# Kernel tuning notes

Measured on AMD Instinct MI355X. Metric: run time of the kernel, lower is better.

## Reference

```python
import jax, jax.numpy as jnp
import numpy as np

SOC, EOS = 3, 2
NUM_HEADS = 12
LN_EPS = 1e-5


def setup_inputs() -> dict:
    key = jax.random.key(0)
    ks = jax.random.split(key, 24)
    B, S, D, N, FF, K = 8, 4096, 768, 1024, 3072, 640
    img = jax.random.normal(ks[0], (B, N, D), jnp.float32)
    hid = jax.random.normal(ks[1], (B, S, D), jnp.float32)
    seq = jax.random.randint(ks[2], (B, S), 4, 100)
    m = jax.random.uniform(ks[3], (B, S)) < 0.125
    seq = jnp.where(m, SOC, seq).at[:, 0].set(SOC)  # ensure >=1 SOC per row
    w = lambda k, a, b: jax.random.normal(k, (a, b), jnp.float32) * 0.02
    return {
        "img": img, "hid": hid, "seq": seq,
        "wq_s": w(ks[4], D, D), "wk_s": w(ks[5], D, D), "wv_s": w(ks[6], D, D), "wo_s": w(ks[7], D, D),
        "wq_c": w(ks[8], D, D), "wk_c": w(ks[9], D, D), "wv_c": w(ks[10], D, D), "wo_c": w(ks[11], D, D),
        "w_ff1": w(ks[12], D, FF), "w_ff2": w(ks[13], FF, D),
        "ln1_s": jnp.ones((D,)), "ln1_b": jnp.zeros((D,)),
        "ln2_s": jnp.ones((D,)), "ln2_b": jnp.zeros((D,)),
        "ln3_s": jnp.ones((D,)), "ln3_b": jnp.zeros((D,)),
        "cap": K,
    }


def _ln(x, s, b):
    mu = jnp.mean(x, axis=-1, keepdims=True)
    var = jnp.var(x, axis=-1, keepdims=True)
    return (x - mu) * jax.lax.rsqrt(var + LN_EPS) * s + b


def _mha(q_in, kv_in, wq, wk, wv, wo, key_mask):
    # q_in [B,Lq,D], kv_in [B,Lk,D], key_mask [B,Lk] bool or None
    B, Lq, D = q_in.shape
    H = NUM_HEADS
    dh = D // H
    q = (q_in @ wq).reshape(B, Lq, H, dh)
    k = (kv_in @ wk).reshape(B, -1, H, dh)
    v = (kv_in @ wv).reshape(B, -1, H, dh)
    scores = jnp.einsum("bqhd,bkhd->bhqk", q, k) / np.sqrt(dh).astype(q.dtype)
    if key_mask is not None:
        scores = jnp.where(key_mask[:, None, None, :], scores, jnp.asarray(-1e9, scores.dtype))
    att = jax.nn.softmax(scores, axis=-1)
    out = jnp.einsum("bhqk,bkhd->bqhd", att, v).reshape(B, Lq, D)
    return out @ wo


def _extract(data, mask, cap):
    # data [B,S,...], mask [B,S] bool -> packed+zero-padded [B,cap,...]
    pos = jnp.cumsum(mask, axis=1) - 1          # slot for each valid token
    pos = jnp.where(mask, pos, cap)             # invalid tokens -> dump slot
    def one(d, p):
        buf = jnp.zeros((cap + 1,) + d.shape[1:], d.dtype)
        return buf.at[p].set(d)[:cap]
        # note: dump slot cap is sliced away
    return jax.vmap(one)(data, pos), pos


def reference(img, hid, seq, wq_s, wk_s, wv_s, wo_s, wq_c, wk_c, wv_c, wo_c,
              w_ff1, w_ff2, ln1_s, ln1_b, ln2_s, ln2_b, ln3_s, ln3_b, cap):
    # mask: SOC tokens occurring before the first EOS
    soc = (seq == SOC) & (jnp.cumsum(seq == EOS, axis=1) == 0)  # [B,S]
    ext, pos = _extract(hid, soc, cap)                          # [B,K,D]
    counts = jnp.sum(soc, axis=1)                               # [B]
    run = jnp.arange(cap)[None, :] < counts[:, None]            # [B,K] valid slots

    # Blocks: pre-LN self-attn (key mask = run), cross-attn to img, FFN
    x = ext
    x = x + _mha(_ln(x, ln1_s, ln1_b), _ln(x, ln1_s, ln1_b), wq_s, wk_s, wv_s, wo_s, run)
    x = x + _mha(_ln(x, ln2_s, ln2_b), img, wq_c, wk_c, wv_c, wo_c, None)
    h = _ln(x, ln3_s, ln3_b)
    x = x + jax.nn.gelu(h @ w_ff1) @ w_ff2

    # masked_scatter back: each SOC position (b,s) takes x[b, pos[b,s]]
    idx = jnp.clip(pos, 0, cap - 1)
    gathered = jnp.take_along_axis(x, idx[:, :, None], axis=1)  # [B,S,D]
    hid_new = jnp.where(soc[:, :, None], gathered, hid)
    return hid_new, x
```

## Files before the change

### kernel.cpp

```cpp
#include <hip/hip_runtime.h>
#include <hip/hip_bf16.h>


#define B_    8
#define S_    4096
#define D_    768
#define N_    1024
#define FF_   3072
#define H_    12
#define DH_   64
#define KCAP  640
#define SOC_TOK 3
#define EOS_TOK 2

typedef __hip_bfloat16 bf16;
typedef unsigned short u16;
typedef __attribute__((ext_vector_type(8))) short short8;
typedef __attribute__((ext_vector_type(4))) float f32x4;

__device__ __forceinline__ u16 ftou16(float x){ union{bf16 b; u16 s;} c; c.b = __float2bfloat16(x); return c.s; }
__device__ __forceinline__ unsigned pk2(float lo, float hi){ return (unsigned)ftou16(lo) | ((unsigned)ftou16(hi)<<16); }

__device__ __forceinline__ f32x4 MFMA(short8 a, short8 b, f32x4 c){
  return __builtin_amdgcn_mfma_f32_16x16x32_bf16(a, b, c, 0, 0, 0);
}

__device__ __forceinline__ void gld16(const void* gp, void* lp){
  __builtin_amdgcn_global_load_lds(
    reinterpret_cast<const __attribute__((address_space(1))) unsigned int*>((size_t)gp),
    reinterpret_cast<__attribute__((address_space(3))) unsigned int*>((size_t)lp),
    16, 0, 0);
}

template<int N> __device__ __forceinline__ void vwait(){
  asm volatile("s_waitcnt vmcnt(%0)" :: "i"(N) : "memory");
}
__device__ __forceinline__ void wgbar(){ asm volatile("s_barrier" ::: "memory"); }

__device__ __forceinline__ int xcd_swz(){
  int id = blockIdx.x;
  return (id & 7) * ((int)gridDim.x >> 3) + (id >> 3);
}

__device__ void scan_body(const int* __restrict__ seq, int* __restrict__ pos,
                          int* __restrict__ src, int* __restrict__ counts, int b){
  int tid = threadIdx.x;
  __shared__ int sd[256];
  __shared__ int carryE, carryS;
  if (tid==0){ carryE=0; carryS=0; }
  __syncthreads();
  for (int c=0; c<S_; c+=256){
    int s   = c + tid;
    int tok = seq[b*S_ + s];
    int isE = (tok==EOS_TOK) ? 1 : 0;
    int isS = (tok==SOC_TOK) ? 1 : 0;
    sd[tid]=isE; __syncthreads();
    for (int off=1; off<256; off<<=1){ int t_=(tid>=off)?sd[tid-off]:0; __syncthreads(); sd[tid]+=t_; __syncthreads(); }
    int eIncl = sd[tid];
    int eTot  = sd[255];
    int valid = (isS && (carryE + eIncl)==0) ? 1 : 0;
    __syncthreads();
    sd[tid]=valid; __syncthreads();
    for (int off=1; off<256; off<<=1){ int t_=(tid>=off)?sd[tid-off]:0; __syncthreads(); sd[tid]+=t_; __syncthreads(); }
    int vIncl = sd[tid];
    int vTot  = sd[255];
    if (valid){
      int slot = carryS + vIncl - 1;
      pos[b*S_ + s] = slot;
      if (slot < KCAP) src[b*KCAP + slot] = s;
    } else {
      pos[b*S_ + s] = -1;
    }
    __syncthreads();
    if (tid==0){ carryE += eTot; carryS += vTot; }
    __syncthreads();
  }
  if (tid==0) counts[b] = (carryS < KCAP) ? carryS : KCAP;
}

struct TransArgs { const float* w[10]; u16* o[10]; };
__global__ __launch_bounds__(256) void transpose_scan_k(TransArgs a, const int* __restrict__ seq,
                                                        int* __restrict__ pos, int* __restrict__ src,
                                                        int* __restrict__ counts,
                                                        const float* __restrict__ img, u16* __restrict__ imgB){
  int id = blockIdx.x;
  if (id >= 9224){
    int base = (id - 9224)*2048 + threadIdx.x*8;
    float4 a0 = *(const float4*)(img + base);
    float4 a1 = *(const float4*)(img + base + 4);
    uint4 wv;
    wv.x = pk2(a0.x,a0.y); wv.y = pk2(a0.z,a0.w); wv.z = pk2(a1.x,a1.y); wv.w = pk2(a1.z,a1.w);
    *(uint4*)(imgB + base) = wv;
    return;
  }
  if (id >= 9216){ scan_body(seq, pos, src, counts, id - 9216); return; }
  __shared__ float tile[32][33];
  int wi, t, K, N;
  if (id < 4608){ wi = id/576; t = id%576; K = 768; N = 768; }
  else if (id < 6912){ wi = 8; t = id-4608; K = 768; N = 3072; }
  else { wi = 9; t = id-6912; K = 3072; N = 768; }
  const float* in = a.w[wi]; u16* out = a.o[wi];
  int nbx = N >> 5;
  int bx = t % nbx, by = t / nbx;
  int tx = threadIdx.x & 31, ty = threadIdx.x >> 5;
  #pragma unroll
  for (int i=0;i<4;++i)
    tile[ty + i*8][tx] = in[(size_t)(by*32 + ty + i*8)*N + bx*32 + tx];
  __syncthreads();
  #pragma unroll
  for (int i=0;i<4;++i)
    out[(size_t)(bx*32 + ty + i*8)*K + by*32 + tx] = ftou16(tile[tx][ty + i*8]);
}

__global__ __launch_bounds__(256) void gather_ln_k(const float* __restrict__ hid,
                                                   const int* __restrict__ src,
                                                   const int* __restrict__ counts,
                                                   const float* __restrict__ g, const float* __restrict__ bt,
                                                   float* __restrict__ X, u16* __restrict__ T0){
  int bk = blockIdx.x; int b = bk / KCAP; int k = bk % KCAP;
  int tid = threadIdx.x;
  float v0, v1, v2;
  if (k < counts[b]){
    const float* hr = hid + ((size_t)b*S_ + src[b*KCAP + k])*D_;
    v0 = hr[tid]; v1 = hr[tid+256]; v2 = hr[tid+512];
  } else { v0 = v1 = v2 = 0.f; }
  float* xr = X + (size_t)bk*D_;
  xr[tid] = v0; xr[tid+256] = v1; xr[tid+512] = v2;
  float s1=v0+v1+v2, s2=v0*v0+v1*v1+v2*v2;
  for (int off=32; off; off>>=1){ s1+=__shfl_xor(s1,off); s2+=__shfl_xor(s2,off); }
  __shared__ float red[8];
  __shared__ float mu_s, rs_s;
  int w=tid>>6, ln=tid&63;
  if (ln==0){ red[w]=s1; red[4+w]=s2; }
  __syncthreads();
  if (tid==0){
    float S1=red[0]+red[1]+red[2]+red[3];
    float S2=red[4]+red[5]+red[6]+red[7];
    float mu = S1*(1.f/D_);
    float var= S2*(1.f/D_) - mu*mu;
    mu_s=mu; rs_s=rsqrtf(var + 1e-5f);
  }
  __syncthreads();
  float mu=mu_s, rs=rs_s;
  u16* yr = T0 + (size_t)bk*D_;
  yr[tid]     = ftou16((v0-mu)*rs*g[tid]     + bt[tid]);
  yr[tid+256] = ftou16((v1-mu)*rs*g[tid+256] + bt[tid+256]);
  yr[tid+512] = ftou16((v2-mu)*rs*g[tid+512] + bt[tid+512]);
}

__global__ __launch_bounds__(256) void ln_k(const float* __restrict__ X, u16* __restrict__ Y,
                                            const float* __restrict__ g, const float* __restrict__ bt){
  int r = blockIdx.x; int tid = threadIdx.x;
  const float* xr = X + (size_t)r*D_;
  float v0=xr[tid], v1=xr[tid+256], v2=xr[tid+512];
  float s1=v0+v1+v2, s2=v0*v0+v1*v1+v2*v2;
  for (int off=32; off; off>>=1){ s1+=__shfl_xor(s1,off); s2+=__shfl_xor(s2,off); }
  __shared__ float red[8];
  __shared__ float mu_s, rs_s;
  int w=tid>>6, ln=tid&63;
  if (ln==0){ red[w]=s1; red[4+w]=s2; }
  __syncthreads();
  if (tid==0){
    float S1=red[0]+red[1]+red[2]+red[3];
    float S2=red[4]+red[5]+red[6]+red[7];
    float mu = S1*(1.f/D_);
    float var= S2*(1.f/D_) - mu*mu;
    mu_s=mu; rs_s=rsqrtf(var + 1e-5f);
  }
  __syncthreads();
  float mu=mu_s, rs=rs_s;
  u16* yr = Y + (size_t)r*D_;
  yr[tid]     = ftou16((v0-mu)*rs*g[tid]     + bt[tid]);
  yr[tid+256] = ftou16((v1-mu)*rs*g[tid+256] + bt[tid+256]);
  yr[tid+512] = ftou16((v2-mu)*rs*g[tid+512] + bt[tid+512]);
}

template<int MODE, int BM, typename TA>
__device__ __forceinline__ void gemm_body(char* ldsp, const TA* __restrict__ A, const u16* __restrict__ Bt,
                                          void* __restrict__ C0, void* __restrict__ C1, void* __restrict__ C2,
                                          int wgid, int N, int K){
  constexpr int MI   = BM/32;
  constexpr int NBUF = (BM==128) ? 2 : ((sizeof(TA)==4) ? 2 : 3);
  u16* As = (u16*)ldsp;
  u16* Bs = (u16*)(ldsp + NBUF*(BM*32)*2);
  int nbx = N >> 7;
  int bx = wgid % nbx, by = wgid / nbx;
  int tid = threadIdx.x;
  int w = tid>>6, l = tid&63, g = l>>4, c = l&15;
  int wr = w&1, wc = w>>1;
  f32x4 acc[MI][4] = {};
  float4 rg[4];
  const int NK = K/32;

  auto STAGEB = [&](int buf, int kt){
    #pragma unroll
    for (int p=0;p<2;++p){
      int row = w*32 + p*16 + (l>>2);
      int su  = (l&3) ^ ((row>>1)&3);
      gld16((const void*)(Bt + (size_t)(bx*128+row)*K + kt + su*8), (void*)&Bs[buf*128*32 + (w*32+p*16)*32]);
    }
  };
  auto STAGEA16 = [&](int buf, int kt){
    if constexpr (BM==128){
      #pragma unroll
      for (int p=0;p<2;++p){
        int row = w*32 + p*16 + (l>>2);
        int su  = (l&3) ^ ((row>>1)&3);
        gld16((const void*)((const u16*)A + (size_t)(by*BM+row)*K + kt + su*8), (void*)&As[buf*BM*32 + (w*32+p*16)*32]);
      }
    } else {
      int row = w*16 + (l>>2);
      int su  = (l&3) ^ ((row>>1)&3);
      gld16((const void*)((const u16*)A + (size_t)(by*BM+row)*K + kt + su*8), (void*)&As[buf*BM*32 + (w*16)*32]);
    }
  };
  auto LOADREG = [&](int kt){
    if constexpr (BM==128){
      const float* ap = (const float*)A + (size_t)(by*BM + (tid>>1))*K + kt + (tid&1)*16;
      rg[0]=*(const float4*)ap;     rg[1]=*(const float4*)(ap+4);
      rg[2]=*(const float4*)(ap+8); rg[3]=*(const float4*)(ap+12);
    } else {
      const float* ap = (const float*)A + (size_t)(by*BM + (tid>>2))*K + kt + (tid&3)*8;
      rg[0] = *(const float4*)ap; rg[1] = *(const float4*)(ap+4);
    }
  };
  auto WRITEA = [&](int buf){
    if constexpr (BM==128){
      int row = tid>>1, half = tid&1;
      uint4 w0,w1;
      w0.x=pk2(rg[0].x,rg[0].y); w0.y=pk2(rg[0].z,rg[0].w); w0.z=pk2(rg[1].x,rg[1].y); w0.w=pk2(rg[1].z,rg[1].w);
      w1.x=pk2(rg[2].x,rg[2].y); w1.y=pk2(rg[2].z,rg[2].w); w1.z=pk2(rg[3].x,rg[3].y); w1.w=pk2(rg[3].z,rg[3].w);
      int sw = (row>>1)&3;
      *(uint4*)&As[buf*BM*32 + row*32 + ((half*2  )^sw)*8] = w0;
      *(uint4*)&As[buf*BM*32 + row*32 + ((half*2+1)^sw)*8] = w1;
    } else {
      int row = tid>>2, unit = tid&3;
      uint4 wv;
      wv.x=pk2(rg[0].x,rg[0].y); wv.y=pk2(rg[0].z,rg[0].w); wv.z=pk2(rg[1].x,rg[1].y); wv.w=pk2(rg[1].z,rg[1].w);
      int sw = (row>>1)&3;
      *(uint4*)&As[buf*BM*32 + row*32 + (unit^sw)*8] = wv;
    }
  };
  auto COMPUTE = [&](int buf){
    short8 af[MI], bfr[4];
    #pragma unroll
    for (int mi=0;mi<MI;++mi){ int row = wr*(MI*16) + mi*16 + c; af[mi]  = *(const short8*)&As[buf*BM*32 + row*32 + (g^((row>>1)&3))*8]; }
    #pragma unroll
    for (int ni=0;ni<4;++ni){ int row = wc*64 + ni*16 + c;       bfr[ni] = *(const short8*)&Bs[buf*128*32 + row*32 + (g^((row>>1)&3))*8]; }
    #pragma unroll
    for (int mi=0;mi<MI;++mi)
      #pragma unroll
      for (int ni=0;ni<4;++ni) acc[mi][ni] = MFMA(af[mi], bfr[ni], acc[mi][ni]);
  };

  if constexpr (BM==128 || sizeof(TA)==4){
    if constexpr (sizeof(TA)==4){ LOADREG(0); STAGEB(0,0); WRITEA(0); }
    else { STAGEA16(0,0); STAGEB(0,0); }
    __syncthreads();
    int buf = 0;
    for (int t=0;t<NK;++t){
      int ktn = (t+1)*32;
      if constexpr (sizeof(TA)==4){
        if (t+1<NK){ LOADREG(ktn); STAGEB(buf^1, ktn); }
        COMPUTE(buf);
        if (t+1<NK) WRITEA(buf^1);
      } else {
        if (t+1<NK){ STAGEA16(buf^1, ktn); STAGEB(buf^1, ktn); }
        COMPUTE(buf);
      }
      __syncthreads();
      buf ^= 1;
    }
  } else {
    constexpr int LPS = 3;
    STAGEA16(0,0);  STAGEB(0,0);
    STAGEA16(1,32); STAGEB(1,32);
    vwait<LPS>();
    wgbar();
    int buf = 0;
    for (int t=0;t<NK;++t){
      if (t+2 < NK){
        int nb = buf+2; if (nb>=3) nb-=3;
        STAGEA16(nb,(t+2)*32); STAGEB(nb,(t+2)*32);
      }
      COMPUTE(buf);
      if (t < NK-2) vwait<LPS>(); else vwait<0>();
      wgbar();
      ++buf; if (buf==3) buf=0;
    }
  }

  int row0 = by*BM + wr*(MI*16), col0 = bx*128 + wc*64;
  #pragma unroll
  for (int mi=0;mi<MI;++mi)
    #pragma unroll
    for (int ni=0;ni<4;++ni){
      int rowb = row0 + mi*16 + g*4;
      int col  = col0 + ni*16 + c;
      if (MODE==4 && col >= 1536){
        int vv = col - 1536; int bb = rowb / KCAP; int key = rowb - bb*KCAP;
        ushort4 pk;
        pk.x = ftou16(acc[mi][ni][0]); pk.y = ftou16(acc[mi][ni][1]);
        pk.z = ftou16(acc[mi][ni][2]); pk.w = ftou16(acc[mi][ni][3]);
        *(ushort4*)&((u16*)C2)[((size_t)(bb*768 + vv))*KCAP + key] = pk;
      } else if (MODE==5 && col >= 768){
        int vv = col - 768; int bb = rowb >> 10; int key = rowb & 1023;
        ushort4 pk;
        pk.x = ftou16(acc[mi][ni][0]); pk.y = ftou16(acc[mi][ni][1]);
        pk.z = ftou16(acc[mi][ni][2]); pk.w = ftou16(acc[mi][ni][3]);
        *(ushort4*)&((u16*)C2)[((size_t)(bb*768 + vv))*1024 + key] = pk;
      } else {
        #pragma unroll
        for (int r=0;r<4;++r){
          int row = rowb + r;
          float v = acc[mi][ni][r];
          if (MODE==0){
            ((u16*)C0)[(size_t)row*N + col] = ftou16(v);
          } else if (MODE==1){
            ((float*)C0)[(size_t)row*N + col] += v;
          } else if (MODE==2){
            float z2 = 1.5957691216057308f*(v + 0.044715f*v*v*v);
            float e  = __expf(z2);
            float th = 1.f - 2.f/(e + 1.f);
            ((u16*)C0)[(size_t)row*N + col] = ftou16(0.5f*v*(1.f+th));
          } else if (MODE==6){
            size_t idx = (size_t)row*N + col;
            float fin = ((float*)C0)[idx] + v;
            ((float*)C0)[idx] = fin;
            ((float*)C1)[idx] = fin;
          } else if (MODE==4){
            if (col < 768)  ((u16*)C0)[(size_t)row*768 + col]       = ftou16(v);
            else            ((u16*)C1)[(size_t)row*768 + col - 768] = ftou16(v);
          } else {
            ((u16*)C0)[(size_t)row*768 + col] = ftou16(v);
          }
        }
      }
    }
}

template<int MODE, int BM, typename TA>
__global__ __launch_bounds__(256) void gemm_k(const TA* __restrict__ A, const u16* __restrict__ Bt,
                                              void* __restrict__ C0, void* __restrict__ C1, void* __restrict__ C2,
                                              int N, int K){
  constexpr int NBUF = (BM==128) ? 2 : ((sizeof(TA)==4) ? 2 : 3);
  __shared__ __align__(16) char pool[NBUF*(BM+128)*32*2];
  gemm_body<MODE,BM,TA>(pool, A, Bt, C0, C1, C2, xcd_swz(), N, K);
}

__global__ __launch_bounds__(256) void mega1_k(const u16* __restrict__ T0, const u16* __restrict__ wqkv_st,
                                               u16* __restrict__ Qb, u16* __restrict__ Kb, u16* __restrict__ VtS,
                                               const u16* __restrict__ imgB, const u16* __restrict__ wkv_ct,
                                               u16* __restrict__ KbC, u16* __restrict__ VtC){
  __shared__ __align__(16) char pool[2*(128+128)*32*2];
  int wgid = xcd_swz();
  if (wgid < 720) gemm_body<4,128,u16>(pool, T0,   wqkv_st, Qb,  Kb,      VtS, wgid,     2304, 768);
  else            gemm_body<5,128,u16>(pool, imgB, wkv_ct,  KbC, nullptr, VtC, wgid-720, 1536, 768);
}

template<int MASKED>
__global__ __launch_bounds__(256) void attn_k(const u16* __restrict__ Q, const u16* __restrict__ Kb,
                                              const u16* __restrict__ Vt, u16* __restrict__ O,
                                              const int* __restrict__ counts, int Lk){
  __shared__ __align__(16) u16 Ks[3][64*64];
  __shared__ __align__(16) u16 Vs[3][64*64];
  __shared__ __align__(16) u16 P[4][16][72];
  int tid = threadIdx.x;
  int w = tid>>6, l = tid&63, g = l>>4, c = l&15;
  int wgid = xcd_swz();
  int qc = wgid % 5;
  int bh = wgid / 5;
  int h = bh % H_, b = bh / H_;
  int q0 = qc*128 + w*32;
  int cnt = MASKED ? counts[b] : Lk;
  int nt = (cnt + 63) >> 6;

  short8 qf[2][2];
  #pragma unroll
  for (int mi=0;mi<2;++mi){
    const u16* Qrow = Q + ((size_t)(b*KCAP + q0 + mi*16 + c))*D_ + h*DH_;
    qf[mi][0] = *(const short8*)(Qrow + g*8);
    qf[mi][1] = *(const short8*)(Qrow + 32 + g*8);
  }

  int srow8 = (l>>3);
  int sunit = l&7;
  auto STAGE = [&](int buf, int kb){
    #pragma unroll
    for (int p=0;p<2;++p){
      int r0 = w*16 + p*8;
      int rowK = r0 + srow8;
      int su = sunit ^ (rowK&7);
      gld16((const void*)(Kb + ((size_t)(b*Lk + kb + rowK))*D_ + h*DH_ + su*8), (void*)&Ks[buf][r0*64]);
      gld16((const void*)(Vt + ((size_t)(b*D_ + h*DH_ + rowK))*Lk + kb + su*8), (void*)&Vs[buf][r0*64]);
    }
  };

  f32x4 o[2][4] = {};
  float m_[2][4], l_[2][4] = {};
  #pragma unroll
  for (int mi=0;mi<2;++mi)
    #pragma unroll
    for (int r=0;r<4;++r) m_[mi][r] = -1e30f;

  STAGE(0, 0);
  if (nt > 1){ STAGE(1, 64); vwait<4>(); } else { vwait<0>(); }
  wgbar();
  int buf = 0;
  for (int t=0; t<nt; ++t){
    int kb = t*64;
    if (t+2 < nt){
      int nb = buf+2; if (nb>=3) nb-=3;
      STAGE(nb, kb+128);
    }
    short8 fr[4][2];
    #pragma unroll
    for (int nb=0;nb<4;++nb)
      #pragma unroll
      for (int kh=0;kh<2;++kh)
        fr[nb][kh] = *(const short8*)&Ks[buf][(nb*16+c)*64 + (((kh<<2)|g) ^ (c&7))*8];
    f32x4 z[2][4];
    #pragma unroll
    for (int mi=0;mi<2;++mi)
      #pragma unroll
      for (int nb=0;nb<4;++nb){
        f32x4 zz = {0.f,0.f,0.f,0.f};
        zz = MFMA(qf[mi][0], fr[nb][0], zz);
        zz = MFMA(qf[mi][1], fr[nb][1], zz);
        z[mi][nb] = zz;
      }
    float pv[2][4][4];
    #pragma unroll
    for (int nb=0;nb<4;++nb){
      bool msk = MASKED && (kb + nb*16 + c >= cnt);
      #pragma unroll
      for (int mi=0;mi<2;++mi)
        #pragma unroll
        for (int r=0;r<4;++r) pv[mi][nb][r] = msk ? -1e30f : z[mi][nb][r]*0.125f;
    }
    float scl[2][4];
    #pragma unroll
    for (int mi=0;mi<2;++mi){
      #pragma unroll
      for (int r=0;r<4;++r){
        float v = fmaxf(fmaxf(pv[mi][0][r],pv[mi][1][r]), fmaxf(pv[mi][2][r],pv[mi][3][r]));
        v = fmaxf(v, __shfl_xor(v,1)); v = fmaxf(v, __shfl_xor(v,2));
        v = fmaxf(v, __shfl_xor(v,4)); v = fmaxf(v, __shfl_xor(v,8));
        float nm = fmaxf(m_[mi][r], v);
        scl[mi][r] = __expf(m_[mi][r] - nm);
        m_[mi][r] = nm;
      }
      #pragma unroll
      for (int r=0;r<4;++r){
        float acc2 = 0.f;
        #pragma unroll
        for (int nb=0;nb<4;++nb){
          float e = __expf(pv[mi][nb][r] - m_[mi][r]);
          pv[mi][nb][r] = e; acc2 += e;
        }
        acc2 += __shfl_xor(acc2,1); acc2 += __shfl_xor(acc2,2);
        acc2 += __shfl_xor(acc2,4); acc2 += __shfl_xor(acc2,8);
        l_[mi][r] = l_[mi][r]*scl[mi][r] + acc2;
      }
      #pragma unroll
      for (int nbd=0;nbd<4;++nbd)
        #pragma unroll
        for (int r=0;r<4;++r) o[mi][nbd][r] *= scl[mi][r];
    }
    #pragma unroll
    for (int nbd=0;nbd<4;++nbd)
      #pragma unroll
      for (int kh=0;kh<2;++kh)
        fr[nbd][kh] = *(const short8*)&Vs[buf][(nbd*16+c)*64 + (((kh<<2)|g) ^ (c&7))*8];
    #pragma unroll
    for (int mi=0;mi<2;++mi){
      #pragma unroll
      for (int nb=0;nb<4;++nb)
        #pragma unroll
        for (int r=0;r<4;++r) P[w][g*4+r][nb*16+c] = ftou16(pv[mi][nb][r]);
      short8 pa0 = *(const short8*)&P[w][c][g*8];
      short8 pa1 = *(const short8*)&P[w][c][32 + g*8];
      #pragma unroll
      for (int nbd=0;nbd<4;++nbd){
        o[mi][nbd] = MFMA(pa0, fr[nbd][0], o[mi][nbd]);
        o[mi][nbd] = MFMA(pa1, fr[nbd][1], o[mi][nbd]);
      }
    }
    if (t < nt-2) vwait<4>(); else vwait<0>();
    wgbar();
    ++buf; if (buf==3) buf=0;
  }
  #pragma unroll
  for (int mi=0;mi<2;++mi)
    #pragma unroll
    for (int nbd=0;nbd<4;++nbd)
      #pragma unroll
      for (int r=0;r<4;++r)
        O[((size_t)(b*KCAP + q0 + mi*16 + g*4 + r))*D_ + h*DH_ + nbd*16 + c] = ftou16(o[mi][nbd][r] / l_[mi][r]);
}

__global__ __launch_bounds__(256) void scatter_k(const int* __restrict__ pos, const float* __restrict__ X,
                                                 const float* __restrict__ hid, float* __restrict__ out0){
  int bs = blockIdx.x; int tid = threadIdx.x;
  int b = bs >> 12;
  int p = pos[bs];
  float* orow = out0 + (size_t)bs*D_;
  if (p >= 0){
    int pc = p < KCAP ? p : (KCAP-1);
    const float* xr = X + ((size_t)(b*KCAP + pc))*D_;
    orow[tid]     = xr[tid];
    orow[tid+256] = xr[tid+256];
    orow[tid+512] = xr[tid+512];
  } else {
    const float* hr = hid + (size_t)bs*D_;
    orow[tid]     = hr[tid];
    orow[tid+256] = hr[tid+256];
    orow[tid+512] = hr[tid+512];
  }
}

extern "C" void kernel_launch(void* const* d_in, const int* in_sizes, int n_in,
                              void* d_out, int out_size, void* d_ws, size_t ws_size,
                              hipStream_t stream){
  const float* img  = (const float*)d_in[0];
  const float* hid  = (const float*)d_in[1];
  const int*   seq  = (const int*)  d_in[2];
  const float* W[10] = { (const float*)d_in[3], (const float*)d_in[4], (const float*)d_in[5], (const float*)d_in[6],
                         (const float*)d_in[7], (const float*)d_in[8], (const float*)d_in[9], (const float*)d_in[10],
                         (const float*)d_in[11], (const float*)d_in[12] };
  const float* ln1s = (const float*)d_in[13];
  const float* ln1b = (const float*)d_in[14];
  const float* ln2s = (const float*)d_in[15];
  const float* ln2b = (const float*)d_in[16];
  const float* ln3s = (const float*)d_in[17];
  const float* ln3b = (const float*)d_in[18];

  char* ws = (char*)d_ws;
  int*   pos    = (int*)  (ws + 0);
  int*   src    = (int*)  (ws + 131072);
  int*   counts = (int*)  (ws + 151552);
  float* X      = (float*)(ws + 151808);
  u16*   T0     = (u16*)  (ws + 15880448);
  u16*   Qb     = (u16*)  (ws + 23744768);
  u16*   Kb     = (u16*)  (ws + 31609088);
  u16*   VtS    = (u16*)  (ws + 39473408);
  u16*   KbC    = (u16*)  (ws + 47337728);
  u16*   VtC    = (u16*)  (ws + 59920640);
  u16*   AO     = (u16*)  (ws + 72503552);
  u16*   Wt     = (u16*)  (ws + 80367872);
  u16*   MID    = Qb;

  u16* wqkv_st = Wt + 0ull*589824;
  u16* wo_st   = Wt + 3ull*589824;
  u16* wq_ct   = Wt + 4ull*589824;
  u16* wkv_ct  = Wt + 5ull*589824;
  u16* wo_ct   = Wt + 7ull*589824;
  u16* wff1t   = Wt + 8ull*589824;
  u16* wff2t   = wff1t + 2359296;

  float* out0 = (float*)d_out;
  float* out1 = out0 + (size_t)B_*S_*D_;
  u16* imgB = (u16*)out1;

  TransArgs ta;
  for (int i=0;i<10;++i) ta.w[i] = W[i];
  for (int i=0;i<8;++i)  ta.o[i] = Wt + (size_t)i*589824;
  ta.o[8] = wff1t; ta.o[9] = wff2t;

  transpose_scan_k<<<12296, 256, 0, stream>>>(ta, seq, pos, src, counts, img, imgB);
  gather_ln_k<<<B_*KCAP, 256, 0, stream>>>(hid, src, counts, ln1s, ln1b, X, T0);

  const int G_MEGA1 = 720 + 768;
  const int G_N768  = (5120/64)*(768/128);
  const int G_FF1   = (5120/128)*(3072/128);
  const int G_ATT   = B_*H_*5;

  mega1_k<<<G_MEGA1, 256, 0, stream>>>(T0, wqkv_st, Qb, Kb, VtS, imgB, wkv_ct, KbC, VtC);
  attn_k<1><<<G_ATT, 256, 0, stream>>>(Qb, Kb, VtS, AO, counts, KCAP);
  gemm_k<1,64,u16><<<G_N768, 256, 0, stream>>>(AO, wo_st, X, nullptr, nullptr, 768, 768);

  ln_k<<<5120, 256, 0, stream>>>(X, T0, ln2s, ln2b);
  gemm_k<0,64,u16><<<G_N768, 256, 0, stream>>>(T0, wq_ct, Qb, nullptr, nullptr, 768, 768);
  attn_k<0><<<G_ATT, 256, 0, stream>>>(Qb, KbC, VtC, AO, counts, N_);
  gemm_k<1,64,u16><<<G_N768, 256, 0, stream>>>(AO, wo_ct, X, nullptr, nullptr, 768, 768);

  ln_k<<<5120, 256, 0, stream>>>(X, T0, ln3s, ln3b);
  gemm_k<2,128,u16><<<G_FF1, 256, 0, stream>>>(T0, wff1t, MID, nullptr, nullptr, 3072, 768);
  gemm_k<6,64,u16><<<G_N768, 256, 0, stream>>>(MID, wff2t, X, out1, nullptr, 768, 3072);

  scatter_k<<<B_*S_, 256, 0, stream>>>(pos, X, hid, out0);
}
```

Baseline: 427.4 us.

## Halve attention query tile per block and split scatter into early copy plus SOC scatter

Attention blocks now process 64 queries (16 per wave) instead of 128, doubling the grid to 960 blocks so more CUs are busy. This raises occupancy at the cost of reloading each K/V tile twice as often. The non-SOC passthrough copy of hid into the output moves into the early prep kernel, and the final scatter only writes SOC rows, read from out1. The FF2 epilogue now writes only out1 instead of writing both X and out1, saving one store per element.

```diff
diff --git a/kernel.cpp b/kernel.cpp
--- a/kernel.cpp
+++ b/kernel.cpp
@@ -112,13 +112,29 @@
     out[(size_t)(bx*32 + ty + i*8)*K + by*32 + tx] = ftou16(tile[tx][ty + i*8]);
 }
 
-__global__ __launch_bounds__(256) void gather_ln_k(const float* __restrict__ hid,
-                                                   const int* __restrict__ src,
-                                                   const int* __restrict__ counts,
-                                                   const float* __restrict__ g, const float* __restrict__ bt,
-                                                   float* __restrict__ X, u16* __restrict__ T0){
-  int bk = blockIdx.x; int b = bk / KCAP; int k = bk % KCAP;
-  int tid = threadIdx.x;
+__global__ __launch_bounds__(256) void prep_k(const float* __restrict__ hid,
+                                              const int* __restrict__ src,
+                                              const int* __restrict__ counts,
+                                              const int* __restrict__ pos,
+                                              const float* __restrict__ g, const float* __restrict__ bt,
+                                              float* __restrict__ X, u16* __restrict__ T0,
+                                              float* __restrict__ out0){
+  int id = blockIdx.x; int tid = threadIdx.x;
+  if (id >= 5120){
+    int base = (id - 5120)*4;
+    #pragma unroll
+    for (int r2=0;r2<4;++r2){
+      int bs = base + r2;
+      if (pos[bs] >= 0) continue;
+      const float* hr = hid + (size_t)bs*D_;
+      float* orow = out0 + (size_t)bs*D_;
+      orow[tid]     = hr[tid];
+      orow[tid+256] = hr[tid+256];
+      orow[tid+512] = hr[tid+512];
+    }
+    return;
+  }
+  int bk = id; int b = bk / KCAP; int k = bk % KCAP;
   float v0, v1, v2;
   if (k < counts[b]){
     const float* hr = hid + ((size_t)b*S_ + src[b*KCAP + k])*D_;
@@ -325,9 +341,7 @@
             ((u16*)C0)[(size_t)row*N + col] = ftou16(0.5f*v*(1.f+th));
           } else if (MODE==6){
             size_t idx = (size_t)row*N + col;
-            float fin = ((float*)C0)[idx] + v;
-            ((float*)C0)[idx] = fin;
-            ((float*)C1)[idx] = fin;
+            ((float*)C1)[idx] = ((const float*)C0)[idx] + v;
           } else if (MODE==4){
             if (col < 768)  ((u16*)C0)[(size_t)row*768 + col]       = ftou16(v);
             else            ((u16*)C1)[(size_t)row*768 + col - 768] = ftou16(v);
@@ -368,20 +382,16 @@
   int tid = threadIdx.x;
   int w = tid>>6, l = tid&63, g = l>>4, c = l&15;
   int wgid = xcd_swz();
-  int qc = wgid % 5;
-  int bh = wgid / 5;
+  int qc = wgid % 10;
+  int bh = wgid / 10;
   int h = bh % H_, b = bh / H_;
-  int q0 = qc*128 + w*32;
+  int q0 = qc*64 + w*16;
   int cnt = MASKED ? counts[b] : Lk;
   int nt = (cnt + 63) >> 6;
 
-  short8 qf[2][2];
-  #pragma unroll
-  for (int mi=0;mi<2;++mi){
-    const u16* Qrow = Q + ((size_t)(b*KCAP + q0 + mi*16 + c))*D_ + h*DH_;
-    qf[mi][0] = *(const short8*)(Qrow + g*8);
-    qf[mi][1] = *(const short8*)(Qrow + 32 + g*8);
-  }
+  const u16* Qrow = Q + ((size_t)(b*KCAP + q0 + c))*D_ + h*DH_;
+  short8 qf0 = *(const short8*)(Qrow + g*8);
+  short8 qf1 = *(const short8*)(Qrow + 32 + g*8);
 
   int srow8 = (l>>3);
   int sunit = l&7;
@@ -396,12 +406,10 @@
     }
   };
 
-  f32x4 o[2][4] = {};
-  float m_[2][4], l_[2][4] = {};
+  f32x4 o[4] = {};
+  float m_[4], l_[4] = {};
   #pragma unroll
-  for (int mi=0;mi<2;++mi)
-    #pragma unroll
-    for (int r=0;r<4;++r) m_[mi][r] = -1e30f;
+  for (int r=0;r<4;++r) m_[r] = -1e30f;
 
   STAGE(0, 0);
   if (nt > 1){ STAGE(1, 64); vwait<4>(); } else { vwait<0>(); }
@@ -419,103 +427,86 @@
       #pragma unroll
       for (int kh=0;kh<2;++kh)
         fr[nb][kh] = *(const short8*)&Ks[buf][(nb*16+c)*64 + (((kh<<2)|g) ^ (c&7))*8];
-    f32x4 z[2][4];
-    #pragma unroll
-    for (int mi=0;mi<2;++mi)
+    float pv[4][4];
+    #pragma unroll
+    for (int nb=0;nb<4;++nb){
+      f32x4 zz = {0.f,0.f,0.f,0.f};
+      zz = MFMA(qf0, fr[nb][0], zz);
+      zz = MFMA(qf1, fr[nb][1], zz);
+      bool msk = MASKED && (kb + nb*16 + c >= cnt);
+      #pragma unroll
+      for (int r=0;r<4;++r) pv[nb][r] = msk ? -1e30f : zz[r]*0.125f;
+    }
+    float scl[4];
+    #pragma unroll
+    for (int r=0;r<4;++r){
+      float v = fmaxf(fmaxf(pv[0][r],pv[1][r]), fmaxf(pv[2][r],pv[3][r]));
+      v = fmaxf(v, __shfl_xor(v,1)); v = fmaxf(v, __shfl_xor(v,2));
+      v = fmaxf(v, __shfl_xor(v,4)); v = fmaxf(v, __shfl_xor(v,8));
+      float nm = fmaxf(m_[r], v);
+      scl[r] = __expf(m_[r] - nm);
+      m_[r] = nm;
+    }
+    #pragma unroll
+    for (int r=0;r<4;++r){
+      float acc2 = 0.f;
       #pragma unroll
       for (int nb=0;nb<4;++nb){
-        f32x4 zz = {0.f,0.f,0.f,0.f};
-        zz = MFMA(qf[mi][0], fr[nb][0], zz);
-        zz = MFMA(qf[mi][1], fr[nb][1], zz);
-        z[mi][nb] = zz;
+        float e = __expf(pv[nb][r] - m_[r]);
+        pv[nb][r] = e; acc2 += e;
       }
-    float pv[2][4][4];
-    #pragma unroll
-    for (int nb=0;nb<4;++nb){
-      bool msk = MASKED && (kb + nb*16 + c >= cnt);
-      #pragma unroll
-      for (int mi=0;mi<2;++mi)
-        #pragma unroll
-        for (int r=0;r<4;++r) pv[mi][nb][r] = msk ? -1e30f : z[mi][nb][r]*0.125f;
-    }
-    float scl[2][4];
-    #pragma unroll
-    for (int mi=0;mi<2;++mi){
-      #pragma unroll
-      for (int r=0;r<4;++r){
-        float v = fmaxf(fmaxf(pv[mi][0][r],pv[mi][1][r]), fmaxf(pv[mi][2][r],pv[mi][3][r]));
-        v = fmaxf(v, __shfl_xor(v,1)); v = fmaxf(v, __shfl_xor(v,2));
-        v = fmaxf(v, __shfl_xor(v,4)); v = fmaxf(v, __shfl_xor(v,8));
-        float nm = fmaxf(m_[mi][r], v);
-        scl[mi][r] = __expf(m_[mi][r] - nm);
-        m_[mi][r] = nm;
-      }
-      #pragma unroll
-      for (int r=0;r<4;++r){
-        float acc2 = 0.f;
-        #pragma unroll
-        for (int nb=0;nb<4;++nb){
-          float e = __expf(pv[mi][nb][r] - m_[mi][r]);
-          pv[mi][nb][r] = e; acc2 += e;
-        }
-        acc2 += __shfl_xor(acc2,1); acc2 += __shfl_xor(acc2,2);
-        acc2 += __shfl_xor(acc2,4); acc2 += __shfl_xor(acc2,8);
-        l_[mi][r] = l_[mi][r]*scl[mi][r] + acc2;
-      }
-      #pragma unroll
-      for (int nbd=0;nbd<4;++nbd)
-        #pragma unroll
-        for (int r=0;r<4;++r) o[mi][nbd][r] *= scl[mi][r];
+      acc2 += __shfl_xor(acc2,1); acc2 += __shfl_xor(acc2,2);
+      acc2 += __shfl_xor(acc2,4); acc2 += __shfl_xor(acc2,8);
+      l_[r] = l_[r]*scl[r] + acc2;
     }
     #pragma unroll
     for (int nbd=0;nbd<4;++nbd)
       #pragma unroll
+      for (int r=0;r<4;++r) o[nbd][r] *= scl[r];
+    short8 fv[4][2];
+    #pragma unroll
+    for (int nbd=0;nbd<4;++nbd)
+      #pragma unroll
       for (int kh=0;kh<2;++kh)
-        fr[nbd][kh] = *(const short8*)&Vs[buf][(nbd*16+c)*64 + (((kh<<2)|g) ^ (c&7))*8];
-    #pragma unroll
-    for (int mi=0;mi<2;++mi){
-      #pragma unroll
-      for (int nb=0;nb<4;++nb)
-        #pragma unroll
-        for (int r=0;r<4;++r) P[w][g*4+r][nb*16+c] = ftou16(pv[mi][nb][r]);
-      short8 pa0 = *(const short8*)&P[w][c][g*8];
-      short8 pa1 = *(const short8*)&P[w][c][32 + g*8];
-      #pragma unroll
-      for (int nbd=0;nbd<4;++nbd){
-        o[mi][nbd] = MFMA(pa0, fr[nbd][0], o[mi][nbd]);
-        o[mi][nbd] = MFMA(pa1, fr[nbd][1], o[mi][nbd]);
-      }
+        fv[nbd][kh] = *(const short8*)&Vs[buf][(nbd*16+c)*64 + (((kh<<2)|g) ^ (c&7))*8];
+    #pragma unroll
+    for (int nb=0;nb<4;++nb)
+      #pragma unroll
+      for (int r=0;r<4;++r) P[w][g*4+r][nb*16+c] = ftou16(pv[nb][r]);
+    short8 pa0 = *(const short8*)&P[w][c][g*8];
+    short8 pa1 = *(const short8*)&P[w][c][32 + g*8];
+    #pragma unroll
+    for (int nbd=0;nbd<4;++nbd){
+      o[nbd] = MFMA(pa0, fv[nbd][0], o[nbd]);
+      o[nbd] = MFMA(pa1, fv[nbd][1], o[nbd]);
     }
     if (t < nt-2) vwait<4>(); else vwait<0>();
     wgbar();
     ++buf; if (buf==3) buf=0;
   }
   #pragma unroll
-  for (int mi=0;mi<2;++mi)
-    #pragma unroll
-    for (int nbd=0;nbd<4;++nbd)
-      #pragma unroll
-      for (int r=0;r<4;++r)
-        O[((size_t)(b*KCAP + q0 + mi*16 + g*4 + r))*D_ + h*DH_ + nbd*16 + c] = ftou16(o[mi][nbd][r] / l_[mi][r]);
-}
-
-__global__ __launch_bounds__(256) void scatter_k(const int* __restrict__ pos, const float* __restrict__ X,
-                                                 const float* __restrict__ hid, float* __restrict__ out0){
-  int bs = blockIdx.x; int tid = threadIdx.x;
-  int b = bs >> 12;
-  int p = pos[bs];
-  float* orow = out0 + (size_t)bs*D_;
-  if (p >= 0){
+  for (int nbd=0;nbd<4;++nbd)
+    #pragma unroll
+    for (int r=0;r<4;++r)
+      O[((size_t)(b*KCAP + q0 + g*4 + r))*D_ + h*DH_ + nbd*16 + c] = ftou16(o[nbd][r] / l_[r]);
+}
+
+__global__ __launch_bounds__(256) void scatter_soc_k(const int* __restrict__ pos,
+                                                     const float* __restrict__ out1,
+                                                     float* __restrict__ out0){
+  int base = blockIdx.x*4; int tid = threadIdx.x;
+  #pragma unroll
+  for (int r2=0;r2<4;++r2){
+    int bs = base + r2;
+    int p = pos[bs];
+    if (p < 0) continue;
     int pc = p < KCAP ? p : (KCAP-1);
-    const float* xr = X + ((size_t)(b*KCAP + pc))*D_;
+    int b = bs >> 12;
+    const float* xr = out1 + ((size_t)(b*KCAP + pc))*D_;
+    float* orow = out0 + (size_t)bs*D_;
     orow[tid]     = xr[tid];
     orow[tid+256] = xr[tid+256];
     orow[tid+512] = xr[tid+512];
-  } else {
-    const float* hr = hid + (size_t)bs*D_;
-    orow[tid]     = hr[tid];
-    orow[tid+256] = hr[tid+256];
-    orow[tid+512] = hr[tid+512];
   }
 }
 
@@ -568,12 +559,12 @@
   ta.o[8] = wff1t; ta.o[9] = wff2t;
 
   transpose_scan_k<<<12296, 256, 0, stream>>>(ta, seq, pos, src, counts, img, imgB);
-  gather_ln_k<<<B_*KCAP, 256, 0, stream>>>(hid, src, counts, ln1s, ln1b, X, T0);
+  prep_k<<<13312, 256, 0, stream>>>(hid, src, counts, pos, ln1s, ln1b, X, T0, out0);
 
   const int G_MEGA1 = 720 + 768;
   const int G_N768  = (5120/64)*(768/128);
   const int G_FF1   = (5120/128)*(3072/128);
-  const int G_ATT   = B_*H_*5;
+  const int G_ATT   = B_*H_*10;
 
   mega1_k<<<G_MEGA1, 256, 0, stream>>>(T0, wqkv_st, Qb, Kb, VtS, imgB, wkv_ct, KbC, VtC);
   attn_k<1><<<G_ATT, 256, 0, stream>>>(Qb, Kb, VtS, AO, counts, KCAP);
@@ -588,5 +579,5 @@
   gemm_k<2,128,u16><<<G_FF1, 256, 0, stream>>>(T0, wff1t, MID, nullptr, nullptr, 3072, 768);
   gemm_k<6,64,u16><<<G_N768, 256, 0, stream>>>(MID, wff2t, X, out1, nullptr, 768, 3072);
 
-  scatter_k<<<B_*S_, 256, 0, stream>>>(pos, X, hid, out0);
-}
+  scatter_soc_k<<<8192, 256, 0, stream>>>(pos, out1, out0);
+}
```

Result: no change. 421.4 us (-1.4%).
